# Optimization experiments

Hardware: AMD Instinct MI355X
Metric: run time of the kernel (lower is better)

Reference implementation:

```python
import jax, jax.numpy as jnp
import numpy as np

B = 8; L = 1024; DEC_IN = 7; D_MODEL = 512; MARK = 4
D_INNER = 1024; D_STATE = 16; D_CONV = 4; DT_RANK = 32
N_HEADS = 8; N_LAYERS = 2; C_OUT = 7


def silu(x):
    return x * jax.nn.sigmoid(x)


def layer_norm(x, g, b):
    mu = x.mean(-1, keepdims=True)
    var = ((x - mu) ** 2).mean(-1, keepdims=True)
    return (x - mu) * jax.lax.rsqrt(var + 1e-5) * g + b


def pos_embed(length, d):
    pos = jnp.arange(length, dtype=jnp.float32)[:, None]
    div = jnp.exp(jnp.arange(0, d, 2, dtype=jnp.float32) * (-np.log(10000.0) / d))
    pe = jnp.zeros((length, d), jnp.float32)
    pe = pe.at[:, 0::2].set(jnp.sin(pos * div))
    pe = pe.at[:, 1::2].set(jnp.cos(pos * div))
    return pe


def _forward(x_dec, x_mark_dec, token_w, temp_w, in_proj_w, conv_w, conv_b,
             x_proj_w, dt_w, dt_b, A_log, D_skip, out_w_m,
             wq, bq, wk, bk, wv, bv, wo, bo,
             ln1_g, ln1_b, ln2_g, ln2_b, proj_w, proj_b):
    Bb, Ll, _ = x_dec.shape
    # DataEmbedding: circular conv1d(k=3) token embed + sinusoidal pos + timeF linear
    xp = jnp.concatenate([x_dec[:, -1:], x_dec, x_dec[:, :1]], axis=1)
    tok = sum(jnp.einsum('blc,cd->bld', xp[:, k:k + Ll], token_w[k]) for k in range(3))
    x = tok + pos_embed(Ll, D_MODEL)[None] + x_mark_dec @ temp_w
    causal = jnp.triu(jnp.ones((Ll, Ll), bool), 1)
    dh = D_MODEL // N_HEADS
    for i in range(N_LAYERS):
        # ---- Mamba block ----
        xz = x @ in_proj_w[i]                      # [B,L,2*D_INNER]
        u, z = jnp.split(xz, 2, axis=-1)
        up = jnp.pad(u, ((0, 0), (D_CONV - 1, 0), (0, 0)))  # causal depthwise conv
        uc = sum(up[:, k:k + Ll] * conv_w[i][:, k] for k in range(D_CONV)) + conv_b[i]
        uc = silu(uc)
        dbc = uc @ x_proj_w[i]
        dt = dbc[..., :DT_RANK]
        Bm = dbc[..., DT_RANK:DT_RANK + D_STATE]
        Cm = dbc[..., DT_RANK + D_STATE:]
        delta = jax.nn.softplus(dt @ dt_w[i] + dt_b[i])     # [B,L,D_INNER]
        A = -jnp.exp(A_log[i])                              # [D_INNER,D_STATE]

        def step(h, inp):
            d_t, B_t, C_t, u_t = inp                        # [B,di],[B,ds],[B,ds],[B,di]
            h = jnp.exp(d_t[..., None] * A) * h + (d_t * u_t)[..., None] * B_t[:, None, :]
            return h, jnp.einsum('bds,bs->bd', h, C_t)

        h0 = jnp.zeros((Bb, D_INNER, D_STATE), x.dtype)
        xs = (delta.transpose(1, 0, 2), Bm.transpose(1, 0, 2),
              Cm.transpose(1, 0, 2), uc.transpose(1, 0, 2))
        _, ys = jax.lax.scan(step, h0, xs)
        y = ys.transpose(1, 0, 2) + uc * D_skip[i]
        y = y * silu(z)
        x = layer_norm(x + y @ out_w_m[i], ln1_g[i], ln1_b[i])
        # ---- Full causal self-attention ----
        q = (x @ wq[i] + bq[i]).reshape(Bb, Ll, N_HEADS, dh)
        k_ = (x @ wk[i] + bk[i]).reshape(Bb, Ll, N_HEADS, dh)
        v = (x @ wv[i] + bv[i]).reshape(Bb, Ll, N_HEADS, dh)
        scores = jnp.einsum('blhd,bshd->bhls', q, k_) / np.sqrt(dh).astype(np.float32)
        scores = jnp.where(causal, -jnp.inf, scores)
        attn = jax.nn.softmax(scores, axis=-1)
        o = jnp.einsum('bhls,bshd->blhd', attn, v).reshape(Bb, Ll, D_MODEL)
        x = layer_norm(x + o @ wo[i] + bo[i], ln2_g[i], ln2_b[i])
    return x @ proj_w + proj_b


def setup_inputs() -> dict:
    key = jax.random.key(0)
    ks = iter(jax.random.split(key, 48))

    def rn(shape, scale=0.02):
        return jax.random.normal(next(ks), shape, jnp.float32) * scale

    inp = {
        'x_dec': jax.random.normal(next(ks), (B, L, DEC_IN), jnp.float32),
        'x_mark_dec': jax.random.normal(next(ks), (B, L, MARK), jnp.float32),
        'token_w': rn((3, DEC_IN, D_MODEL), 0.1),
        'temp_w': rn((MARK, D_MODEL), 0.1),
        'in_proj_w': rn((N_LAYERS, D_MODEL, 2 * D_INNER)),
        'conv_w': rn((N_LAYERS, D_INNER, D_CONV), 0.1),
        'conv_b': jnp.zeros((N_LAYERS, D_INNER), jnp.float32),
        'x_proj_w': rn((N_LAYERS, D_INNER, DT_RANK + 2 * D_STATE)),
        'dt_w': rn((N_LAYERS, DT_RANK, D_INNER)),
        'dt_b': jnp.full((N_LAYERS, D_INNER), -4.6, jnp.float32),
        'A_log': jnp.tile(jnp.log(jnp.arange(1, D_STATE + 1, dtype=jnp.float32))[None, None, :], (N_LAYERS, D_INNER, 1)),
        'D_skip': jnp.ones((N_LAYERS, D_INNER), jnp.float32),
        'out_w_m': rn((N_LAYERS, D_INNER, D_MODEL)),
        'wq': rn((N_LAYERS, D_MODEL, D_MODEL)),
        'bq': jnp.zeros((N_LAYERS, D_MODEL), jnp.float32),
        'wk': rn((N_LAYERS, D_MODEL, D_MODEL)),
        'bk': jnp.zeros((N_LAYERS, D_MODEL), jnp.float32),
        'wv': rn((N_LAYERS, D_MODEL, D_MODEL)),
        'bv': jnp.zeros((N_LAYERS, D_MODEL), jnp.float32),
        'wo': rn((N_LAYERS, D_MODEL, D_MODEL)),
        'bo': jnp.zeros((N_LAYERS, D_MODEL), jnp.float32),
        'ln1_g': jnp.ones((N_LAYERS, D_MODEL), jnp.float32),
        'ln1_b': jnp.zeros((N_LAYERS, D_MODEL), jnp.float32),
        'ln2_g': jnp.ones((N_LAYERS, D_MODEL), jnp.float32),
        'ln2_b': jnp.zeros((N_LAYERS, D_MODEL), jnp.float32),
        'proj_w': rn((D_MODEL, C_OUT), 0.1),
        'proj_b': jnp.zeros((C_OUT,), jnp.float32),
    }
    return inp


def reference(x_dec, x_mark_dec, token_w, temp_w, in_proj_w, conv_w, conv_b,
              x_proj_w, dt_w, dt_b, A_log, D_skip, out_w_m,
              wq, bq, wk, bk, wv, bv, wo, bo,
              ln1_g, ln1_b, ln2_g, ln2_b, proj_w, proj_b):
    return _forward(x_dec, x_mark_dec, token_w, temp_w, in_proj_w, conv_w, conv_b,
                    x_proj_w, dt_w, dt_b, A_log, D_skip, out_w_m,
                    wq, bq, wk, bk, wv, bv, wo, bo,
                    ln1_g, ln1_b, ln2_g, ln2_b, proj_w, proj_b)
```

## Files before the change

kernel.cpp:

```cpp
#include <hip/hip_runtime.h>
#include <math.h>

#define Bdim 8
#define Ldim 1024
#define DEC_IN 7
#define D_MODEL 512
#define MARK 4
#define D_INNER 1024
#define D_STATE 16
#define D_CONV 4
#define DT_RANK 32
#define N_HEADS 8
#define DH 64
#define ROWS (Bdim*Ldim)
#define MB (1ull<<20)
#define NCHUNK 32
#define CLEN 32

typedef unsigned short u16;
typedef unsigned int u32;
typedef __attribute__((ext_vector_type(8))) short bf16x8;
typedef __attribute__((ext_vector_type(4))) float f32x4;
typedef __attribute__((ext_vector_type(4))) unsigned short u16x4;

__device__ inline float b2f(u16 u) {
    union { u32 i; float f; } c; c.i = ((u32)u) << 16; return c.f;
}
__device__ inline u16 f2b(float f) {
    union { float f; u32 u; } c; c.f = f;
    u32 u = c.u;
    u32 r = (u + 0x7fffu + ((u >> 16) & 1u)) >> 16;
    return (u16)r;
}
__device__ inline void gload16(const void* g, void* l) {
    __builtin_amdgcn_global_load_lds((const __attribute__((address_space(1))) void*)g,
                                     (__attribute__((address_space(3))) void*)l, 16, 0, 0);
}

__global__ void embed_kernel(const float* __restrict__ xd, const float* __restrict__ xmark,
                             const float* __restrict__ token_w, const float* __restrict__ temp_w,
                             float* __restrict__ x, u16* __restrict__ xbf) {
    int bt = blockIdx.x;
    int b = bt >> 10, t = bt & 1023;
    __shared__ float xr[3][DEC_IN];
    __shared__ float mk[MARK];
    if (threadIdx.x < 3*DEC_IN) {
        int k = threadIdx.x / DEC_IN, c = threadIdx.x % DEC_IN;
        int tt = (t + k - 1 + Ldim) % Ldim;
        xr[k][c] = xd[((size_t)b*Ldim + tt)*DEC_IN + c];
    }
    if (threadIdx.x < MARK) mk[threadIdx.x] = xmark[((size_t)b*Ldim + t)*MARK + threadIdx.x];
    __syncthreads();
    for (int dd = threadIdx.x; dd < D_MODEL; dd += 256) {
        float acc = 0.f;
        #pragma unroll
        for (int k = 0; k < 3; ++k)
            #pragma unroll
            for (int c = 0; c < DEC_IN; ++c)
                acc += xr[k][c] * token_w[(k*DEC_IN + c)*D_MODEL + dd];
        int i2 = dd & ~1;
        float freq = expf(-(float)i2 * (logf(10000.f) / (float)D_MODEL));
        float ang = (float)t * freq;
        acc += (dd & 1) ? cosf(ang) : sinf(ang);
        #pragma unroll
        for (int m = 0; m < MARK; ++m) acc += mk[m] * temp_w[m*D_MODEL + dd];
        x[(size_t)bt*D_MODEL + dd] = acc;
        xbf[(size_t)bt*D_MODEL + dd] = f2b(acc);
    }
}

__global__ __launch_bounds__(256) void transpose_cast(const float* __restrict__ W, u16* __restrict__ Wt,
                                                      int K, int N, int srcZ, int dstZ) {
    const float* Wz = W + (size_t)blockIdx.z * srcZ;
    u16* Wtz = Wt + (size_t)blockIdx.z * dstZ;
    __shared__ u16 tile[64][72];
    int k0 = blockIdx.y*64, n0 = blockIdx.x*64;
    int tid = threadIdx.x;
    #pragma unroll
    for (int it = 0; it < 16; ++it) {
        int idx = it*256 + tid; int kr = idx>>6, nc = idx&63;
        tile[kr][nc] = f2b(Wz[(size_t)(k0+kr)*N + n0 + nc]);
    }
    __syncthreads();
    #pragma unroll
    for (int it = 0; it < 2; ++it) {
        int idx = it*256 + tid; int nr = idx>>3, slot = idx&7;
        bf16x8 v;
        #pragma unroll
        for (int j = 0; j < 8; ++j) ((u16*)&v)[j] = tile[slot*8+j][nr];
        *(bf16x8*)(Wtz + (size_t)(n0+nr)*K + k0 + slot*8) = v;
    }
}

__global__ void dtw_transpose(const float* __restrict__ dt_w, u16* __restrict__ dtwT) {
    int idx = blockIdx.x*256 + threadIdx.x;
    int z = idx >> 16, rem = idx & 65535;
    int n = rem >> 6, k = rem & 63;
    dtwT[idx] = (k < 32) ? f2b(dt_w[(size_t)z*32768 + k*1024 + n]) : (u16)0;
}

__global__ void pack_bias(const float* __restrict__ bq, const float* __restrict__ bk,
                          const float* __restrict__ bv, float* __restrict__ dst) {
    int idx = blockIdx.x*256 + threadIdx.x;
    int layer = idx / 1536, c = idx % 1536;
    const float* src = (c < 512) ? bq : (c < 1024) ? bk : bv;
    dst[idx] = src[layer*512 + (c & 511)];
}

template<int OUTMODE, int ACT>
__global__ __launch_bounds__(256) void gemm_bf16(const u16* __restrict__ A, int lda,
                                                 const u16* __restrict__ Bt, int ldb,
                                                 const float* __restrict__ bias, void* __restrict__ Cp,
                                                 int ldc, int gridX, int N, int K,
                                                 u16* __restrict__ vt) {
    __shared__ u16 As[128*64];
    __shared__ u16 Bs[128*64];
    int tid = threadIdx.x;
    int nwg = gridDim.x, q8 = nwg >> 3;
    int bid = blockIdx.x;
    int wg = (bid & 7)*q8 + (bid >> 3);
    int bx = wg % gridX, by = wg / gridX;
    int bm = by*128, bn = bx*128;
    int lane = tid & 63, wv = tid >> 6;
    int rm = (wv & 1)*64, cn = (wv >> 1)*64;
    int l15 = lane & 15, g = lane >> 4;
    int lrow = lane >> 3;
    int lcol = ((lane & 7) ^ lrow) * 8;

    f32x4 acc[4][4] = {};

    for (int k0 = 0; k0 < K; k0 += 64) {
        __syncthreads();
        #pragma unroll
        for (int it = 0; it < 4; ++it) {
            int r0 = wv*32 + it*8;
            gload16(A  + (size_t)(bm + r0 + lrow)*lda + k0 + lcol, As + r0*64);
            gload16(Bt + (size_t)(bn + r0 + lrow)*ldb + k0 + lcol, Bs + r0*64);
        }
        __syncthreads();
        #pragma unroll
        for (int ks = 0; ks < 2; ++ks) {
            bf16x8 af[4], bfr[4];
            #pragma unroll
            for (int m = 0; m < 4; ++m) {
                int row = rm + m*16 + l15;
                af[m]  = *(const bf16x8*)(As + row*64 + (((ks*4+g) ^ (row&7))*8));
                int col = cn + m*16 + l15;
                bfr[m] = *(const bf16x8*)(Bs + col*64 + (((ks*4+g) ^ (col&7))*8));
            }
            #pragma unroll
            for (int m = 0; m < 4; ++m)
                #pragma unroll
                for (int n = 0; n < 4; ++n)
                    acc[m][n] = __builtin_amdgcn_mfma_f32_16x16x32_bf16(af[m], bfr[n], acc[m][n], 0, 0, 0);
        }
    }

    float bv4[4];
    #pragma unroll
    for (int n = 0; n < 4; ++n) bv4[n] = bias ? bias[bn + cn + n*16 + l15] : 0.f;

    #pragma unroll
    for (int m = 0; m < 4; ++m) {
        #pragma unroll
        for (int n = 0; n < 4; ++n) {
            int col = bn + cn + n*16 + l15;
            #pragma unroll
            for (int r = 0; r < 4; ++r) {
                int row = bm + rm + m*16 + g*4 + r;
                float v = acc[m][n][r] + bv4[n];
                if (ACT == 1) v = (v > 20.f) ? v : log1pf(__expf(v));
                if (OUTMODE == 1) {
                    ((u16*)Cp)[(size_t)row*ldc + col] = f2b(v);
                } else {
                    int b = row >> 10, t = row & 1023;
                    if (col < 1024) ((u16*)Cp)[(size_t)row*ldc + col] = f2b(v);
                    else vt[((size_t)(b*D_MODEL) + (col - 1024))*Ldim + t] = f2b(v);
                }
            }
        }
    }
}

__global__ __launch_bounds__(256) void xproj_kernel(const u16* __restrict__ ucb, const u16* __restrict__ xprT,
                                                    float* __restrict__ dbc, u16* __restrict__ dtb) {
    __shared__ u16 As[64*64];
    __shared__ u16 Bs[64*64];
    int tid = threadIdx.x, lane = tid & 63, wv = tid >> 6;
    int l15 = lane & 15, g = lane >> 4;
    int bm = blockIdx.x*64;
    f32x4 acc[4] = {};
    for (int k0 = 0; k0 < 1024; k0 += 64) {
        __syncthreads();
        #pragma unroll
        for (int it = 0; it < 2; ++it) {
            int idx = it*256 + tid; int row = idx >> 3, slot = idx & 7;
            bf16x8 av = *(const bf16x8*)(ucb + (size_t)(bm+row)*1024 + k0 + slot*8);
            *(bf16x8*)((char*)As + row*128 + ((slot ^ (row&7)) << 4)) = av;
            bf16x8 bv = *(const bf16x8*)(xprT + (size_t)row*1024 + k0 + slot*8);
            *(bf16x8*)((char*)Bs + row*128 + ((slot ^ (row&7)) << 4)) = bv;
        }
        __syncthreads();
        #pragma unroll
        for (int ks = 0; ks < 2; ++ks) {
            int arow = wv*16 + l15;
            bf16x8 af = *(const bf16x8*)((const char*)As + arow*128 + (((ks*4+g) ^ (arow&7)) << 4));
            #pragma unroll
            for (int n = 0; n < 4; ++n) {
                int col = n*16 + l15;
                bf16x8 bfr = *(const bf16x8*)((const char*)Bs + col*128 + (((ks*4+g) ^ (col&7)) << 4));
                acc[n] = __builtin_amdgcn_mfma_f32_16x16x32_bf16(af, bfr, acc[n], 0, 0, 0);
            }
        }
    }
    #pragma unroll
    for (int n = 0; n < 4; ++n) {
        int col = n*16 + l15;
        #pragma unroll
        for (int r = 0; r < 4; ++r) {
            int row = bm + wv*16 + g*4 + r;
            float v = acc[n][r];
            dbc[(size_t)row*64 + col] = v;
            dtb[(size_t)row*64 + col] = (col < 32) ? f2b(v) : (u16)0;
        }
    }
}

__global__ __launch_bounds__(256) void proj_kernel(const float* __restrict__ x, const float* __restrict__ w,
                                                   const float* __restrict__ pb, float* __restrict__ out) {
    int row = blockIdx.x*4 + (threadIdx.x >> 6);
    int lane = threadIdx.x & 63;
    const float* xr = x + (size_t)row*D_MODEL + lane*8;
    float xv[8];
    #pragma unroll
    for (int j = 0; j < 8; ++j) xv[j] = xr[j];
    const float* wr = w + lane*56;
    float acc[7] = {0,0,0,0,0,0,0};
    #pragma unroll
    for (int j = 0; j < 8; ++j)
        #pragma unroll
        for (int c = 0; c < 7; ++c) acc[c] = fmaf(xv[j], wr[j*7 + c], acc[c]);
    #pragma unroll
    for (int c = 0; c < 7; ++c) {
        #pragma unroll
        for (int off = 32; off; off >>= 1) acc[c] += __shfl_xor(acc[c], off);
    }
    if (lane < 7) out[(size_t)row*7 + lane] = acc[lane] + pb[lane];
}

__global__ void conv_silu_kernel(const u16* __restrict__ xz, const float* __restrict__ conv_w,
                                 const float* __restrict__ conv_b, u16* __restrict__ ucb) {
    int idx = blockIdx.x*256 + threadIdx.x;
    int d8 = idx & 127, bt = idx >> 7;
    int t = bt & 1023, b = bt >> 10;
    int d0 = d8*8;
    float4 cb0 = *(const float4*)(conv_b + d0);
    float4 cb1 = *(const float4*)(conv_b + d0 + 4);
    float acc[8] = {cb0.x,cb0.y,cb0.z,cb0.w, cb1.x,cb1.y,cb1.z,cb1.w};
    float w[8][4];
    #pragma unroll
    for (int j = 0; j < 8; ++j) *(float4*)&w[j][0] = *(const float4*)(conv_w + (d0+j)*4);
    #pragma unroll
    for (int k = 0; k < 4; ++k) {
        int tt = t + k - 3;
        if (tt >= 0) {
            bf16x8 v = *(const bf16x8*)(xz + ((size_t)(b*Ldim + tt))*2048 + d0);
            #pragma unroll
            for (int j = 0; j < 8; ++j)
                acc[j] = fmaf(b2f(((u16*)&v)[j]), w[j][k], acc[j]);
        }
    }
    bf16x8 o;
    #pragma unroll
    for (int j = 0; j < 8; ++j) {
        float s = acc[j] / (1.f + __expf(-acc[j]));
        ((u16*)&o)[j] = f2b(s);
    }
    *(bf16x8*)(ucb + (size_t)bt*1024 + d0) = o;
}

__global__ __launch_bounds__(256) void scan_part1(const u16* __restrict__ delta,
                                                  const u16* __restrict__ ucb,
                                                  const float* __restrict__ dbc,
                                                  const float* __restrict__ A_log,
                                                  float* __restrict__ hend,
                                                  float* __restrict__ aprod) {
    int c = blockIdx.y;
    int bd = blockIdx.x*256 + threadIdx.x;
    int d = bd & 1023, b = bd >> 10;
    float A[D_STATE], h[D_STATE], ap[D_STATE];
    #pragma unroll
    for (int s = 0; s < D_STATE; ++s) { A[s] = -__expf(A_log[d*D_STATE + s]); h[s] = 0.f; ap[s] = 1.f; }
    const u16*   dptr = delta + (size_t)b*Ldim*D_INNER + d;
    const u16*   uptr = ucb   + (size_t)b*Ldim*D_INNER + d;
    const float* bc   = dbc   + (size_t)b*Ldim*64;
    for (int tt = 0; tt < CLEN; ++tt) {
        int t = c*CLEN + tt;
        float dl = b2f(dptr[(size_t)t*D_INNER]);
        float ut = b2f(uptr[(size_t)t*D_INNER]);
        float du = dl * ut;
        float4 b0 = *(const float4*)(bc + t*64 + 32);
        float4 b1 = *(const float4*)(bc + t*64 + 36);
        float4 b2 = *(const float4*)(bc + t*64 + 40);
        float4 b3 = *(const float4*)(bc + t*64 + 44);
        float Bv[16] = {b0.x,b0.y,b0.z,b0.w, b1.x,b1.y,b1.z,b1.w,
                        b2.x,b2.y,b2.z,b2.w, b3.x,b3.y,b3.z,b3.w};
        #pragma unroll
        for (int s = 0; s < D_STATE; ++s) {
            float e = __expf(dl * A[s]);
            h[s] = fmaf(e, h[s], du * Bv[s]);
            ap[s] *= e;
        }
    }
    size_t o = ((size_t)c*ROWS + bd)*D_STATE;
    #pragma unroll
    for (int q = 0; q < 4; ++q) {
        *(float4*)(hend  + o + q*4) = make_float4(h[q*4],  h[q*4+1],  h[q*4+2],  h[q*4+3]);
        *(float4*)(aprod + o + q*4) = make_float4(ap[q*4], ap[q*4+1], ap[q*4+2], ap[q*4+3]);
    }
}

__global__ __launch_bounds__(256) void scan_part2(float* __restrict__ hend,
                                                  const float* __restrict__ aprod) {
    int idx = blockIdx.x*256 + threadIdx.x;
    float hin = 0.f;
    #pragma unroll
    for (int c = 0; c < NCHUNK; ++c) {
        size_t o = (size_t)c*ROWS*D_STATE + idx;
        float he = hend[o], ap = aprod[o];
        hend[o] = hin;
        hin = fmaf(ap, hin, he);
    }
}

__global__ __launch_bounds__(256) void scan_part3(const u16* __restrict__ delta,
                                                  const u16* __restrict__ ucb,
                                                  const float* __restrict__ dbc,
                                                  const float* __restrict__ A_log,
                                                  const float* __restrict__ hend,
                                                  const u16* __restrict__ xz,
                                                  const float* __restrict__ Dskip,
                                                  u16* __restrict__ ysb) {
    int c = blockIdx.y;
    int bd = blockIdx.x*256 + threadIdx.x;
    int d = bd & 1023, b = bd >> 10;
    float A[D_STATE], h[D_STATE];
    size_t o = ((size_t)c*ROWS + bd)*D_STATE;
    #pragma unroll
    for (int s = 0; s < D_STATE; ++s) {
        A[s] = -__expf(A_log[d*D_STATE + s]);
        h[s] = hend[o + s];
    }
    float Dk = Dskip[d];
    const u16*   dptr = delta + (size_t)b*Ldim*D_INNER + d;
    const u16*   uptr = ucb   + (size_t)b*Ldim*D_INNER + d;
    const float* bc   = dbc   + (size_t)b*Ldim*64;
    const u16*   zp   = xz    + (size_t)b*Ldim*2048 + 1024 + d;
    u16* yp = ysb + (size_t)b*Ldim*D_INNER + d;
    for (int tt = 0; tt < CLEN; ++tt) {
        int t = c*CLEN + tt;
        float dl = b2f(dptr[(size_t)t*D_INNER]);
        float ut = b2f(uptr[(size_t)t*D_INNER]);
        float du = dl * ut;
        float4 b0 = *(const float4*)(bc + t*64 + 32);
        float4 b1 = *(const float4*)(bc + t*64 + 36);
        float4 b2 = *(const float4*)(bc + t*64 + 40);
        float4 b3 = *(const float4*)(bc + t*64 + 44);
        float4 c0 = *(const float4*)(bc + t*64 + 48);
        float4 c1 = *(const float4*)(bc + t*64 + 52);
        float4 c2 = *(const float4*)(bc + t*64 + 56);
        float4 c3 = *(const float4*)(bc + t*64 + 60);
        float Bv[16] = {b0.x,b0.y,b0.z,b0.w, b1.x,b1.y,b1.z,b1.w,
                        b2.x,b2.y,b2.z,b2.w, b3.x,b3.y,b3.z,b3.w};
        float Cv[16] = {c0.x,c0.y,c0.z,c0.w, c1.x,c1.y,c1.z,c1.w,
                        c2.x,c2.y,c2.z,c2.w, c3.x,c3.y,c3.z,c3.w};
        float y = 0.f;
        #pragma unroll
        for (int s = 0; s < D_STATE; ++s) {
            float e = __expf(dl * A[s]);
            h[s] = fmaf(e, h[s], du * Bv[s]);
            y = fmaf(h[s], Cv[s], y);
        }
        float z = b2f(zp[(size_t)t*2048]);
        float yy = fmaf(ut, Dk, y);
        yp[(size_t)t*D_INNER] = f2b(yy * (z / (1.f + __expf(-z))));
    }
}

__global__ __launch_bounds__(256) void ln_kernel(float* __restrict__ x, const u16* __restrict__ t,
                                                 const float* __restrict__ g, const float* __restrict__ bta,
                                                 u16* __restrict__ xbf) {
    int row = blockIdx.x * 4 + (threadIdx.x >> 6);
    int lane = threadIdx.x & 63;
    const float* xr = x + (size_t)row*D_MODEL;
    const u16*   tr = t + (size_t)row*D_MODEL;
    float v[8];
    float sum = 0.f;
    #pragma unroll
    for (int j = 0; j < 8; ++j) { v[j] = xr[lane + j*64] + b2f(tr[lane + j*64]); sum += v[j]; }
    #pragma unroll
    for (int off = 32; off; off >>= 1) sum += __shfl_xor(sum, off);
    float mu = sum * (1.f/512.f);
    float vs = 0.f;
    #pragma unroll
    for (int j = 0; j < 8; ++j) { float dm = v[j] - mu; vs += dm*dm; }
    #pragma unroll
    for (int off = 32; off; off >>= 1) vs += __shfl_xor(vs, off);
    float inv = rsqrtf(vs * (1.f/512.f) + 1e-5f);
    #pragma unroll
    for (int j = 0; j < 8; ++j) {
        int c = lane + j*64;
        float o = (v[j] - mu) * inv * g[c] + bta[c];
        x[(size_t)row*D_MODEL + c] = o;
        xbf[(size_t)row*D_MODEL + c] = f2b(o);
    }
}

__global__ __launch_bounds__(256) void attn_mfma(const u16* __restrict__ qk,
                                                 const u16* __restrict__ vt, u16* __restrict__ ob) {
    int bx = blockIdx.x, h = blockIdx.y, b = blockIdx.z;
    int tid = threadIdx.x, lane = tid & 63, w = tid >> 6;
    int l15 = lane & 15, g = lane >> 4;
    __shared__ u16 Ks[32*64];
    __shared__ u16 Vs[64*40];
    __shared__ u16 Ps[4][16*40];
    int qbase = bx*64;
    int qrow = qbase + w*16 + l15;

    const u16* qptr = qk + ((size_t)(b*Ldim + qrow))*1024 + h*DH + g*8;
    bf16x8 qf[2];
    qf[0] = *(const bf16x8*)(qptr);
    qf[1] = *(const bf16x8*)(qptr + 32);

    f32x4 o_acc[4] = {};
    float m_run = -INFINITY, l_run = 0.f;
    int ntiles = bx*2 + 2;

    for (int kt = 0; kt < ntiles; ++kt) {
        __syncthreads();
        {
            int row = tid >> 3, slot = tid & 7;
            bf16x8 v = *(const bf16x8*)(qk + ((size_t)(b*Ldim + kt*32 + row))*1024 + 512 + h*DH + slot*8);
            *(bf16x8*)((char*)Ks + row*128 + ((slot ^ (row&7)) << 4)) = v;
        }
        {
            int row = tid >> 2, slot = tid & 3;
            bf16x8 v = *(const bf16x8*)(vt + ((size_t)(b*D_MODEL + h*DH + row))*Ldim + kt*32 + slot*8);
            *(bf16x8*)((char*)Vs + row*80 + slot*16) = v;
        }
        __syncthreads();

        f32x4 sf[2];
        #pragma unroll
        for (int f = 0; f < 2; ++f) {
            f32x4 a = {0.f, 0.f, 0.f, 0.f};
            #pragma unroll
            for (int ks = 0; ks < 2; ++ks) {
                int row = f*16 + l15;
                bf16x8 kf = *(const bf16x8*)((const char*)Ks + row*128 + (((ks*4+g) ^ (row&7)) << 4));
                a = __builtin_amdgcn_mfma_f32_16x16x32_bf16(kf, qf[ks], a, 0, 0, 0);
            }
            sf[f] = a;
        }

        float pmax = -INFINITY;
        #pragma unroll
        for (int f = 0; f < 2; ++f)
            #pragma unroll
            for (int r = 0; r < 4; ++r) {
                int key = kt*32 + f*16 + g*4 + r;
                float sv = (key <= qrow) ? sf[f][r]*0.125f : -INFINITY;
                sf[f][r] = sv;
                pmax = fmaxf(pmax, sv);
            }
        pmax = fmaxf(pmax, __shfl_xor(pmax, 16));
        pmax = fmaxf(pmax, __shfl_xor(pmax, 32));
        float mnew = fmaxf(m_run, pmax);
        float corr = __expf(m_run - mnew);

        float ps = 0.f;
        #pragma unroll
        for (int f = 0; f < 2; ++f) {
            float p0 = __expf(sf[f][0] - mnew), p1 = __expf(sf[f][1] - mnew);
            float p2 = __expf(sf[f][2] - mnew), p3 = __expf(sf[f][3] - mnew);
            ps += p0 + p1 + p2 + p3;
            u16x4 pk; pk.x = f2b(p0); pk.y = f2b(p1); pk.z = f2b(p2); pk.w = f2b(p3);
            *(u16x4*)((char*)&Ps[w][0] + l15*80 + f*32 + g*8) = pk;
        }
        ps += __shfl_xor(ps, 16);
        ps += __shfl_xor(ps, 32);
        l_run = l_run * corr + ps;
        m_run = mnew;
        #pragma unroll
        for (int t = 0; t < 4; ++t) o_acc[t] *= corr;

        bf16x8 pf = *(const bf16x8*)((const char*)&Ps[w][0] + l15*80 + g*16);
        #pragma unroll
        for (int t = 0; t < 4; ++t) {
            int row = t*16 + l15;
            bf16x8 vf = *(const bf16x8*)((const char*)Vs + row*80 + g*16);
            o_acc[t] = __builtin_amdgcn_mfma_f32_16x16x32_bf16(vf, pf, o_acc[t], 0, 0, 0);
        }
    }

    float invl = 1.f / l_run;
    #pragma unroll
    for (int t = 0; t < 4; ++t) {
        u16x4 o4;
        o4.x = f2b(o_acc[t][0]*invl); o4.y = f2b(o_acc[t][1]*invl);
        o4.z = f2b(o_acc[t][2]*invl); o4.w = f2b(o_acc[t][3]*invl);
        *(u16x4*)(ob + ((size_t)(b*Ldim + qrow))*D_MODEL + h*DH + t*16 + g*4) = o4;
    }
}

extern "C" void kernel_launch(void* const* d_in, const int* in_sizes, int n_in,
                              void* d_out, int out_size, void* d_ws, size_t ws_size,
                              hipStream_t stream) {
    const float* x_dec   = (const float*)d_in[0];
    const float* x_mark  = (const float*)d_in[1];
    const float* token_w = (const float*)d_in[2];
    const float* temp_w  = (const float*)d_in[3];
    const float* in_proj_w = (const float*)d_in[4];
    const float* conv_w  = (const float*)d_in[5];
    const float* conv_b  = (const float*)d_in[6];
    const float* x_proj_w = (const float*)d_in[7];
    const float* dt_w    = (const float*)d_in[8];
    const float* dt_b    = (const float*)d_in[9];
    const float* A_log   = (const float*)d_in[10];
    const float* D_skip  = (const float*)d_in[11];
    const float* out_w_m = (const float*)d_in[12];
    const float* wq = (const float*)d_in[13];
    const float* bq = (const float*)d_in[14];
    const float* wk = (const float*)d_in[15];
    const float* bk = (const float*)d_in[16];
    const float* wv = (const float*)d_in[17];
    const float* bv = (const float*)d_in[18];
    const float* wo = (const float*)d_in[19];
    const float* bo = (const float*)d_in[20];
    const float* ln1_g = (const float*)d_in[21];
    const float* ln1_b = (const float*)d_in[22];
    const float* ln2_g = (const float*)d_in[23];
    const float* ln2_b = (const float*)d_in[24];
    const float* proj_w = (const float*)d_in[25];
    const float* proj_b = (const float*)d_in[26];

    if (ws_size < 160*MB) return;

    char* wsb = (char*)d_ws;
    float* x     = (float*)(wsb + 0);
    u16*   xbf   = (u16*)(wsb + 16*MB);
    u16*   xzb   = (u16*)(wsb + 24*MB);
    u16*   qk    = (u16*)(wsb + 24*MB);
    u16*   obf   = (u16*)(wsb + 40*MB);
    u16*   vtb   = (u16*)(wsb + 56*MB);
    u16*   ucb   = (u16*)(wsb + 64*MB);
    float* hend  = (float*)(wsb + 80*MB);
    float* aprod = (float*)(wsb + 96*MB);
    float* dbc   = (float*)(wsb + 112*MB);
    u16*   dtb   = (u16*)(wsb + 114*MB);
    u16*   delta = (u16*)(wsb + 115*MB);
    u16*   tmp   = delta;
    u16*   ysb   = (u16*)(wsb + 131*MB);
    u16*   iprT  = (u16*)(wsb + 147*MB);
    u16*   outT  = (u16*)(wsb + 151*MB);
    u16*   qkvT  = (u16*)(wsb + 153*MB);
    u16*   oT    = (u16*)(wsb + 156*MB);
    u16*   xprT  = (u16*)(wsb + 157*MB);
    u16*   dtwT  = (u16*)(wsb + 158*MB);
    float* biasP = (float*)(wsb + 159*MB);
    float* out   = (float*)d_out;

    transpose_cast<<<dim3(32, 8, 2), 256, 0, stream>>>(in_proj_w, iprT, 512, 2048, 512*2048, 512*2048);
    transpose_cast<<<dim3(8, 16, 2), 256, 0, stream>>>(out_w_m, outT, 1024, 512, 1024*512, 1024*512);
    transpose_cast<<<dim3(8, 8, 2), 256, 0, stream>>>(wq, qkvT,          512, 512, 512*512, 1536*512);
    transpose_cast<<<dim3(8, 8, 2), 256, 0, stream>>>(wk, qkvT + 512*512, 512, 512, 512*512, 1536*512);
    transpose_cast<<<dim3(8, 8, 2), 256, 0, stream>>>(wv, qkvT + 1024*512, 512, 512, 512*512, 1536*512);
    transpose_cast<<<dim3(8, 8, 2), 256, 0, stream>>>(wo, oT, 512, 512, 512*512, 512*512);
    transpose_cast<<<dim3(1, 16, 2), 256, 0, stream>>>(x_proj_w, xprT, 1024, 64, 1024*64, 1024*64);
    dtw_transpose<<<512, 256, 0, stream>>>(dt_w, dtwT);
    pack_bias<<<12, 256, 0, stream>>>(bq, bk, bv, biasP);

    embed_kernel<<<ROWS, 256, 0, stream>>>(x_dec, x_mark, token_w, temp_w, x, xbf);

    for (int i = 0; i < 2; ++i) {
        gemm_bf16<1,0><<<1024, 256, 0, stream>>>(xbf, 512, iprT + (size_t)i*2048*512, 512,
                                                 nullptr, xzb, 2048, 16, 2048, 512, nullptr);
        conv_silu_kernel<<<(ROWS*128)/256, 256, 0, stream>>>(xzb, conv_w + i*D_INNER*D_CONV,
                                                             conv_b + i*D_INNER, ucb);
        xproj_kernel<<<ROWS/64, 256, 0, stream>>>(ucb, xprT + (size_t)i*64*1024, dbc, dtb);
        gemm_bf16<1,1><<<512, 256, 0, stream>>>(dtb, 64, dtwT + (size_t)i*1024*64, 64,
                                                dt_b + i*D_INNER, delta, 1024, 8, 1024, 64, nullptr);
        scan_part1<<<dim3(32, NCHUNK), 256, 0, stream>>>(delta, ucb, dbc, A_log + i*D_INNER*D_STATE,
                                                         hend, aprod);
        scan_part2<<<(ROWS*D_STATE)/256, 256, 0, stream>>>(hend, aprod);
        scan_part3<<<dim3(32, NCHUNK), 256, 0, stream>>>(delta, ucb, dbc, A_log + i*D_INNER*D_STATE,
                                                         hend, xzb, D_skip + i*D_INNER, ysb);
        gemm_bf16<1,0><<<256, 256, 0, stream>>>(ysb, 1024, outT + (size_t)i*512*1024, 1024,
                                                nullptr, tmp, 512, 4, 512, 1024, nullptr);
        ln_kernel<<<ROWS/4, 256, 0, stream>>>(x, tmp, ln1_g + i*512, ln1_b + i*512, xbf);
        gemm_bf16<3,0><<<768, 256, 0, stream>>>(xbf, 512, qkvT + (size_t)i*1536*512, 512,
                                                biasP + i*1536, qk, 1024, 12, 1536, 512, vtb);
        attn_mfma<<<dim3(Ldim/64, N_HEADS, Bdim), 256, 0, stream>>>(qk, vtb, obf);
        gemm_bf16<1,0><<<256, 256, 0, stream>>>(obf, 512, oT + (size_t)i*512*512, 512,
                                                bo + i*512, tmp, 512, 4, 512, 512, nullptr);
        ln_kernel<<<ROWS/4, 256, 0, stream>>>(x, tmp, ln2_g + i*512, ln2_b + i*512, xbf);
    }
    proj_kernel<<<ROWS/4, 256, 0, stream>>>(x, proj_w, proj_b, out);
}
```

Before: 813.8 us.

## Pair causal attention query tiles per block and enlarge key tiles

Each attention block now handles two query tiles, qt and 15-qt, so causal work is balanced across the 512 blocks instead of ranging from small to large. Key/value tiles grow from 32 to 64 keys, which halves the number of barrier-separated loads per tile. The online-softmax rescale is skipped unless the running max grows by more than a threshold, which saves exp and multiply work but lets probabilities exceed 1 before normalization. The number of blocks is halved, which may reduce occupancy and latency hiding, and larger shared tiles raise LDS use per block.

```diff
diff --git a/kernel.cpp b/kernel.cpp
--- a/kernel.cpp
+++ b/kernel.cpp
@@ -418,98 +418,108 @@
 
 __global__ __launch_bounds__(256) void attn_mfma(const u16* __restrict__ qk,
                                                  const u16* __restrict__ vt, u16* __restrict__ ob) {
-    int bx = blockIdx.x, h = blockIdx.y, b = blockIdx.z;
+    int h = blockIdx.y, b = blockIdx.z;
     int tid = threadIdx.x, lane = tid & 63, w = tid >> 6;
     int l15 = lane & 15, g = lane >> 4;
-    __shared__ u16 Ks[32*64];
-    __shared__ u16 Vs[64*40];
-    __shared__ u16 Ps[4][16*40];
-    int qbase = bx*64;
-    int qrow = qbase + w*16 + l15;
-
-    const u16* qptr = qk + ((size_t)(b*Ldim + qrow))*1024 + h*DH + g*8;
-    bf16x8 qf[2];
-    qf[0] = *(const bf16x8*)(qptr);
-    qf[1] = *(const bf16x8*)(qptr + 32);
-
-    f32x4 o_acc[4] = {};
-    float m_run = -INFINITY, l_run = 0.f;
-    int ntiles = bx*2 + 2;
-
-    for (int kt = 0; kt < ntiles; ++kt) {
-        __syncthreads();
-        {
-            int row = tid >> 3, slot = tid & 7;
-            bf16x8 v = *(const bf16x8*)(qk + ((size_t)(b*Ldim + kt*32 + row))*1024 + 512 + h*DH + slot*8);
-            *(bf16x8*)((char*)Ks + row*128 + ((slot ^ (row&7)) << 4)) = v;
-        }
-        {
-            int row = tid >> 2, slot = tid & 3;
-            bf16x8 v = *(const bf16x8*)(vt + ((size_t)(b*D_MODEL + h*DH + row))*Ldim + kt*32 + slot*8);
-            *(bf16x8*)((char*)Vs + row*80 + slot*16) = v;
-        }
-        __syncthreads();
-
-        f32x4 sf[2];
-        #pragma unroll
-        for (int f = 0; f < 2; ++f) {
-            f32x4 a = {0.f, 0.f, 0.f, 0.f};
+    __shared__ u16 Ks[64*64];
+    __shared__ u16 Vs[64*72];
+    __shared__ u16 Ps[4][16*72];
+
+    #pragma unroll
+    for (int half = 0; half < 2; ++half) {
+        int qt = (half == 0) ? (int)blockIdx.x : 15 - (int)blockIdx.x;
+        int qrow = qt*64 + w*16 + l15;
+        const u16* qptr = qk + ((size_t)(b*Ldim + qrow))*1024 + h*DH + g*8;
+        bf16x8 qf0 = *(const bf16x8*)(qptr);
+        bf16x8 qf1 = *(const bf16x8*)(qptr + 32);
+
+        f32x4 o_acc[4] = {};
+        float m_run = -INFINITY, l_run = 0.f;
+        int ntiles = qt + 1;
+
+        for (int kt = 0; kt < ntiles; ++kt) {
+            __syncthreads();
+            #pragma unroll
+            for (int it = 0; it < 2; ++it) {
+                int idx = it*256 + tid; int row = idx >> 3, slot = idx & 7;
+                bf16x8 v = *(const bf16x8*)(qk + ((size_t)(b*Ldim + kt*64 + row))*1024 + 512 + h*DH + slot*8);
+                *(bf16x8*)((char*)Ks + row*128 + ((slot ^ (row&7)) << 4)) = v;
+            }
+            #pragma unroll
+            for (int it = 0; it < 2; ++it) {
+                int idx = it*256 + tid; int row = idx >> 3, slot = idx & 7;
+                bf16x8 v = *(const bf16x8*)(vt + ((size_t)(b*D_MODEL + h*DH + row))*Ldim + kt*64 + slot*8);
+                *(bf16x8*)((char*)Vs + row*144 + slot*16) = v;
+            }
+            __syncthreads();
+
+            f32x4 sf[4];
+            #pragma unroll
+            for (int f = 0; f < 4; ++f) {
+                f32x4 a = {0.f, 0.f, 0.f, 0.f};
+                int row = f*16 + l15;
+                bf16x8 kf0 = *(const bf16x8*)((const char*)Ks + row*128 + ((g ^ (row&7)) << 4));
+                a = __builtin_amdgcn_mfma_f32_16x16x32_bf16(kf0, qf0, a, 0, 0, 0);
+                bf16x8 kf1 = *(const bf16x8*)((const char*)Ks + row*128 + (((4+g) ^ (row&7)) << 4));
+                a = __builtin_amdgcn_mfma_f32_16x16x32_bf16(kf1, qf1, a, 0, 0, 0);
+                sf[f] = a;
+            }
+
+            float pmax = -INFINITY;
+            #pragma unroll
+            for (int f = 0; f < 4; ++f)
+                #pragma unroll
+                for (int r = 0; r < 4; ++r) {
+                    int key = kt*64 + f*16 + g*4 + r;
+                    float sv = (key <= qrow) ? sf[f][r]*0.125f : -INFINITY;
+                    sf[f][r] = sv;
+                    pmax = fmaxf(pmax, sv);
+                }
+            pmax = fmaxf(pmax, __shfl_xor(pmax, 16));
+            pmax = fmaxf(pmax, __shfl_xor(pmax, 32));
+
+            if (!__all(pmax - m_run <= 8.f)) {
+                float mnew = fmaxf(m_run, pmax);
+                float corr = __expf(m_run - mnew);
+                l_run *= corr;
+                #pragma unroll
+                for (int t = 0; t < 4; ++t) o_acc[t] *= corr;
+                m_run = mnew;
+            }
+
+            float ps = 0.f;
+            #pragma unroll
+            for (int f = 0; f < 4; ++f) {
+                float p0 = __expf(sf[f][0] - m_run), p1 = __expf(sf[f][1] - m_run);
+                float p2 = __expf(sf[f][2] - m_run), p3 = __expf(sf[f][3] - m_run);
+                ps += p0 + p1 + p2 + p3;
+                u16x4 pk; pk.x = f2b(p0); pk.y = f2b(p1); pk.z = f2b(p2); pk.w = f2b(p3);
+                *(u16x4*)((char*)&Ps[w][0] + l15*144 + f*32 + g*8) = pk;
+            }
+            ps += __shfl_xor(ps, 16);
+            ps += __shfl_xor(ps, 32);
+            l_run += ps;
+
             #pragma unroll
             for (int ks = 0; ks < 2; ++ks) {
-                int row = f*16 + l15;
-                bf16x8 kf = *(const bf16x8*)((const char*)Ks + row*128 + (((ks*4+g) ^ (row&7)) << 4));
-                a = __builtin_amdgcn_mfma_f32_16x16x32_bf16(kf, qf[ks], a, 0, 0, 0);
-            }
-            sf[f] = a;
-        }
-
-        float pmax = -INFINITY;
-        #pragma unroll
-        for (int f = 0; f < 2; ++f)
-            #pragma unroll
-            for (int r = 0; r < 4; ++r) {
-                int key = kt*32 + f*16 + g*4 + r;
-                float sv = (key <= qrow) ? sf[f][r]*0.125f : -INFINITY;
-                sf[f][r] = sv;
-                pmax = fmaxf(pmax, sv);
-            }
-        pmax = fmaxf(pmax, __shfl_xor(pmax, 16));
-        pmax = fmaxf(pmax, __shfl_xor(pmax, 32));
-        float mnew = fmaxf(m_run, pmax);
-        float corr = __expf(m_run - mnew);
-
-        float ps = 0.f;
-        #pragma unroll
-        for (int f = 0; f < 2; ++f) {
-            float p0 = __expf(sf[f][0] - mnew), p1 = __expf(sf[f][1] - mnew);
-            float p2 = __expf(sf[f][2] - mnew), p3 = __expf(sf[f][3] - mnew);
-            ps += p0 + p1 + p2 + p3;
-            u16x4 pk; pk.x = f2b(p0); pk.y = f2b(p1); pk.z = f2b(p2); pk.w = f2b(p3);
-            *(u16x4*)((char*)&Ps[w][0] + l15*80 + f*32 + g*8) = pk;
-        }
-        ps += __shfl_xor(ps, 16);
-        ps += __shfl_xor(ps, 32);
-        l_run = l_run * corr + ps;
-        m_run = mnew;
-        #pragma unroll
-        for (int t = 0; t < 4; ++t) o_acc[t] *= corr;
-
-        bf16x8 pf = *(const bf16x8*)((const char*)&Ps[w][0] + l15*80 + g*16);
+                bf16x8 pf = *(const bf16x8*)((const char*)&Ps[w][0] + l15*144 + ks*64 + g*16);
+                #pragma unroll
+                for (int t = 0; t < 4; ++t) {
+                    int row = t*16 + l15;
+                    bf16x8 vf = *(const bf16x8*)((const char*)Vs + row*144 + ks*64 + g*16);
+                    o_acc[t] = __builtin_amdgcn_mfma_f32_16x16x32_bf16(vf, pf, o_acc[t], 0, 0, 0);
+                }
+            }
+        }
+
+        float invl = 1.f / l_run;
         #pragma unroll
         for (int t = 0; t < 4; ++t) {
-            int row = t*16 + l15;
-            bf16x8 vf = *(const bf16x8*)((const char*)Vs + row*80 + g*16);
-            o_acc[t] = __builtin_amdgcn_mfma_f32_16x16x32_bf16(vf, pf, o_acc[t], 0, 0, 0);
-        }
-    }
-
-    float invl = 1.f / l_run;
-    #pragma unroll
-    for (int t = 0; t < 4; ++t) {
-        u16x4 o4;
-        o4.x = f2b(o_acc[t][0]*invl); o4.y = f2b(o_acc[t][1]*invl);
-        o4.z = f2b(o_acc[t][2]*invl); o4.w = f2b(o_acc[t][3]*invl);
-        *(u16x4*)(ob + ((size_t)(b*Ldim + qrow))*D_MODEL + h*DH + t*16 + g*4) = o4;
+            u16x4 o4;
+            o4.x = f2b(o_acc[t][0]*invl); o4.y = f2b(o_acc[t][1]*invl);
+            o4.z = f2b(o_acc[t][2]*invl); o4.w = f2b(o_acc[t][3]*invl);
+            *(u16x4*)(ob + ((size_t)(b*Ldim + qrow))*D_MODEL + h*DH + t*16 + g*4) = o4;
+        }
     }
 }
 
@@ -600,7 +610,7 @@
         ln_kernel<<<ROWS/4, 256, 0, stream>>>(x, tmp, ln1_g + i*512, ln1_b + i*512, xbf);
         gemm_bf16<3,0><<<768, 256, 0, stream>>>(xbf, 512, qkvT + (size_t)i*1536*512, 512,
                                                 biasP + i*1536, qk, 1024, 12, 1536, 512, vtb);
-        attn_mfma<<<dim3(Ldim/64, N_HEADS, Bdim), 256, 0, stream>>>(qk, vtb, obf);
+        attn_mfma<<<dim3(8, N_HEADS, Bdim), 256, 0, stream>>>(qk, vtb, obf);
         gemm_bf16<1,0><<<256, 256, 0, stream>>>(obf, 512, oT + (size_t)i*512*512, 512,
                                                 bo + i*512, tmp, 512, 4, 512, 512, nullptr);
         ln_kernel<<<ROWS/4, 256, 0, stream>>>(x, tmp, ln2_g + i*512, ln2_b + i*512, xbf);
```

Result: slower. 830.7 us (+2.1%).
